# Kernel optimization log

Measured on AMD Instinct MI355X. Metric: run time of the kernel, lower is better.

## Reference

```python
import jax, jax.numpy as jnp
import numpy as np

PAD = 0  # module-level global in the original repo (MT convention)


def setup_inputs() -> dict:
    key = jax.random.key(0)
    k1, k2, k3 = jax.random.split(key, 3)
    N, V, D = 2048, 32000, 512
    # realistic log-probabilities over the vocab
    pred_ll = jax.nn.log_softmax(jax.random.normal(k1, (N, V), jnp.float32), axis=-1)
    target = jax.random.randint(k2, (N,), 0, V)
    # frozen pretrained word-vector table (nn.Embedding.from_pretrained)
    emb = jax.random.normal(k3, (V, D), jnp.float32)
    return {"pred_ll": pred_ll, "target": target, "emb": emb}


def reference(pred_ll, target, emb):
    # pred_ll: [N, V] log-probs; target: [N] int ids; emb: [V, D] frozen table
    mask = (target != PAD).astype(pred_ll.dtype)  # [N] non-pad mask

    # nll_loss = -pred_ll.gather(-1, target) summed over non-pad tokens
    nll = -jnp.take_along_axis(pred_ll, target[:, None], axis=-1)[:, 0]  # [N]
    nll_loss = jnp.sum(nll * mask)

    # pairwise L2 distance gold-embedding vs full table, via the GEMM identity
    # ||g - e||^2 = ||g||^2 + ||e||^2 - 2 g.e  (avoids the [N, V, D] tensor)
    g = emb[target]                                    # [N, D]
    g2 = jnp.sum(g * g, axis=-1, keepdims=True)        # [N, 1]
    e2 = jnp.sum(emb * emb, axis=-1)[None, :]          # [1, V]
    d2 = jnp.maximum(g2 + e2 - 2.0 * (g @ emb.T), 0.0)  # [N, V]
    dist = jnp.sqrt(jnp.maximum(d2, 1e-12))             # [N, V], L2 distances

    dist_max = jnp.max(dist, axis=1, keepdims=True)    # [N, 1]
    w = jax.nn.softmax(dist_max - jnp.abs(dist), axis=1)  # [N, V]

    # loss = sum_v softmax_weight * (-log p), summed over non-pad tokens
    loss = jnp.sum(w * (-pred_ll), axis=1)             # [N]
    return (jnp.sum(loss * mask), nll_loss)
```

## Files before the change

kernel.cpp:

```cpp
#include <hip/hip_runtime.h>
#include <float.h>

#define NTOK   2048
#define VOCAB  32000
#define DIM    512
#define NCHUNK 50
#define NT16   2000
#define TPC    (NT16 / NCHUNK)
#define VCHUNK (VOCAB / NCHUNK)
#define ROWSB  64
#define NRB    (NTOK / ROWSB)
#define TILE_BYTES 8192

typedef __attribute__((ext_vector_type(4))) float f32x4;
typedef unsigned int u32;
typedef long long i64;

__device__ __forceinline__ i64 pack_fp8x8(f32x4 x0, f32x4 x1) {
    int lo = __builtin_amdgcn_cvt_pk_fp8_f32(x0.x, x0.y, 0, false);
    lo = __builtin_amdgcn_cvt_pk_fp8_f32(x0.z, x0.w, lo, true);
    int hi = __builtin_amdgcn_cvt_pk_fp8_f32(x1.x, x1.y, 0, false);
    hi = __builtin_amdgcn_cvt_pk_fp8_f32(x1.z, x1.w, hi, true);
    return (i64)(((unsigned long long)(u32)hi << 32) | (u32)lo);
}

__device__ __forceinline__ void async_copy16(void* lds, const void* g) {
    __builtin_amdgcn_global_load_lds(
        (const __attribute__((address_space(1))) u32*)(const u32*)g,
        (__attribute__((address_space(3))) u32*)(u32*)lds, 16, 0, 0);
}

__global__ void init_out(float* out) {
    if (threadIdx.x < 2) out[threadIdx.x] = 0.f;
}

__global__ __launch_bounds__(256) void precast_kernel(
    const float* __restrict__ emb, char* __restrict__ Bbf, float* __restrict__ e2) {
    const int tile = blockIdx.x;
    const int t = threadIdx.x, w = t >> 6, l = t & 63;
    const int v0 = tile * 16;
    char* tbase = Bbf + (size_t)tile * TILE_BYTES;
    #pragma unroll
    for (int it = 0; it < 4; ++it) {
        const int v = it * 4 + w;
        const float* src = emb + (size_t)(v0 + v) * DIM + l * 8;
        f32x4 x0 = *(const f32x4*)src;
        f32x4 x1 = *(const f32x4*)(src + 4);
        float sq = x0.x*x0.x + x0.y*x0.y + x0.z*x0.z + x0.w*x0.w
                 + x1.x*x1.x + x1.y*x1.y + x1.z*x1.z + x1.w*x1.w;
        #pragma unroll
        for (int m = 1; m < 64; m <<= 1) sq += __shfl_xor(sq, m);
        if (l == 0) e2[v0 + v] = sq;
        *(i64*)(tbase + (l >> 2) * 512 + ((l & 3) * 16 + v) * 8) = pack_fp8x8(x0, x1);
    }
}

__global__ __launch_bounds__(256) void e2_kernel(const float* __restrict__ emb,
                                                 float* __restrict__ e2) {
    int gid = blockIdx.x * 256 + threadIdx.x;
    int wid = gid >> 6, l = gid & 63;
    if (wid >= VOCAB) return;
    const float* row = emb + (size_t)wid * DIM + l * 8;
    f32x4 a = *(const f32x4*)row;
    f32x4 b = *(const f32x4*)(row + 4);
    float s = a.x*a.x + a.y*a.y + a.z*a.z + a.w*a.w
            + b.x*b.x + b.y*b.y + b.z*b.z + b.w*b.w;
    #pragma unroll
    for (int m = 1; m < 64; m <<= 1) s += __shfl_xor(s, m);
    if (l == 0) e2[wid] = s;
}

template<bool PRECAST>
__global__ __launch_bounds__(256, 4) void fused_kernel(
    const float* __restrict__ pred_ll, const int* __restrict__ target,
    const float* __restrict__ emb, const char* __restrict__ Bbf,
    const float* __restrict__ e2g,
    float* __restrict__ partials ) {

    const int rb = blockIdx.x;
    const int ch = blockIdx.y;
    const int t  = threadIdx.x;
    const int w  = t >> 6;
    const int l  = t & 63;
    const int l15 = l & 15;
    const int lg  = l >> 4;

    __shared__ __align__(16) char  ldsB[3][TILE_BYTES];
    __shared__ __align__(16) char  ldsQ[3][4096];
    __shared__ __align__(16) float e2l[VCHUNK];

    const int t0 = ch * TPC, tend = t0 + TPC;
    const int v0base = ch * VCHUNK;
    const int rowblk = rb * ROWSB;
    const int rowbase = rowblk + w * 16;

    i64 afrag[16];
    {
        const int grow = target[rowbase + l15];
        if constexpr (PRECAST) {
            const char* ab = Bbf + (size_t)(grow >> 4) * TILE_BYTES
                           + ((l & 48) + (grow & 15)) * 8;
            #pragma unroll
            for (int ks = 0; ks < 16; ++ks)
                afrag[ks] = *(const i64*)(ab + ks * 512);
        } else {
            const float* gsrc = emb + (size_t)grow * DIM;
            #pragma unroll
            for (int ks = 0; ks < 16; ++ks) {
                const int k0 = ks * 32 + ((l >> 4) << 3);
                afrag[ks] = pack_fp8x8(*(const f32x4*)(gsrc + k0),
                                       *(const f32x4*)(gsrc + k0 + 4));
            }
        }
    }
    float g2[4];
    #pragma unroll
    for (int r = 0; r < 4; ++r) g2[r] = e2g[target[rowbase + lg * 4 + r]];

    float s_[4] = {0.f, 0.f, 0.f, 0.f};
    float ac_[4] = {0.f, 0.f, 0.f, 0.f};

    auto stageF = [&](int buf, int tg) {
        if constexpr (PRECAST) {
            const char* srcB = Bbf + (size_t)tg * TILE_BYTES;
            async_copy16(ldsB[buf] + t * 16, srcB + t * 16);
            async_copy16(ldsB[buf] + 4096 + t * 16, srcB + 4096 + t * 16);
        } else {
            #pragma unroll
            for (int it = 0; it < 4; ++it) {
                const int slot = it * 256 + t;
                const int ks = slot >> 6, il = slot & 63;
                const int v = il & 15, k0 = ks * 32 + ((il >> 4) << 3);
                const float* src = emb + (size_t)(tg * 16 + v) * DIM + k0;
                *(i64*)(ldsB[buf] + ks * 512 + il * 8) =
                    pack_fp8x8(*(const f32x4*)src, *(const f32x4*)(src + 4));
            }
        }
        const float* srcQ = pred_ll + (size_t)(rowblk + (t >> 2)) * VOCAB
                          + tg * 16 + (t & 3) * 4;
        async_copy16(ldsQ[buf] + t * 16, srcQ);
    };

    if (t < VCHUNK / 4) async_copy16(e2l + t * 4, e2g + v0base + t * 4);
    stageF(0, t0);
    stageF(1, t0 + 1);

    int ibr = 0;
    #pragma unroll 1
    for (int tg = t0; tg < tend; ++tg) {
        if (tg == tend - 1) {
            asm volatile("s_waitcnt vmcnt(0)" ::: "memory");
        } else {
            if constexpr (PRECAST)
                asm volatile("s_waitcnt vmcnt(3)" ::: "memory");
            else
                asm volatile("s_waitcnt vmcnt(1) lgkmcnt(0)" ::: "memory");
        }
        __builtin_amdgcn_s_barrier();
        __builtin_amdgcn_sched_barrier(0);

        const int ibw = (ibr >= 1) ? ibr - 1 : ibr + 2;
        if (tg + 2 < tend) stageF(ibw, tg + 2);

        f32x4 acc = {0.f, 0.f, 0.f, 0.f};
        const char* lb = ldsB[ibr];
        #pragma unroll
        for (int ks = 0; ks < 16; ++ks) {
            const i64 b = *(const i64*)(lb + ks * 512 + l * 8);
            acc = __builtin_amdgcn_mfma_f32_16x16x32_fp8_fp8(afrag[ks], b, acc, 0, 0, 0);
        }

        const float e2v = e2l[(tg - t0) * 16 + l15];
        const char* lq = ldsQ[ibr];
        #pragma unroll
        for (int r = 0; r < 4; ++r) {
            const float q = *(const float*)(lq + ((w * 16 + lg * 4 + r) * 64 + l15 * 4));
            float d2 = fmaxf(fmaf(-2.f, acc[r], g2[r] + e2v), 1e-12f);
            const float e = __expf(-sqrtf(d2));
            s_[r] += e;
            ac_[r] = fmaf(e, -q, ac_[r]);
        }

        ibr = (ibr >= 2) ? 0 : ibr + 1;
    }

    #pragma unroll
    for (int r = 0; r < 4; ++r) {
        float sv = s_[r], av = ac_[r];
        #pragma unroll
        for (int m = 1; m < 16; m <<= 1) {
            sv += __shfl_xor(sv, m);
            av += __shfl_xor(av, m);
        }
        if (l15 == 0) {
            const int rg = rowbase + lg * 4 + r;
            float* pp = partials + ((size_t)rg * NCHUNK + ch) * 2;
            pp[0] = sv; pp[1] = av;
        }
    }
}

__global__ __launch_bounds__(256) void reduce_kernel(
    const float* __restrict__ pred_ll, const int* __restrict__ target,
    const float* __restrict__ partials, float* __restrict__ out) {
    const int row = blockIdx.x * 256 + threadIdx.x;
    float loss = 0.f, nll = 0.f;
    if (row < NTOK) {
        const int tg = target[row];
        const float mask = (tg != 0) ? 1.f : 0.f;
        const float* pp = partials + (size_t)row * NCHUNK * 2;
        float S = 0.f, A = 0.f;
        #pragma unroll 5
        for (int c = 0; c < NCHUNK; ++c) { S += pp[c * 2]; A += pp[c * 2 + 1]; }
        loss = mask * (A / S);
        nll  = mask * (-pred_ll[(size_t)row * VOCAB + tg]);
    }
    #pragma unroll
    for (int o = 32; o > 0; o >>= 1) {
        loss += __shfl_xor(loss, o);
        nll  += __shfl_xor(nll, o);
    }
    if ((threadIdx.x & 63) == 0) {
        atomicAdd(&out[0], loss);
        atomicAdd(&out[1], nll);
    }
}

extern "C" void kernel_launch(void* const* d_in, const int* in_sizes, int n_in,
                              void* d_out, int out_size, void* d_ws, size_t ws_size,
                              hipStream_t stream) {
    const float* pred_ll = (const float*)d_in[0];
    const int*   target  = (const int*)d_in[1];
    const float* emb     = (const float*)d_in[2];
    float* out = (float*)d_out;

    float* e2       = (float*)d_ws;
    float* partials = e2 + VOCAB;
    const size_t base = (size_t)VOCAB * 4 + (size_t)NTOK * NCHUNK * 2 * 4;
    char* Bbf       = (char*)d_ws + base;
    const size_t need = base + (size_t)NT16 * TILE_BYTES;
    const bool precast = (ws_size >= need);

    hipLaunchKernelGGL(init_out, dim3(1), dim3(64), 0, stream, out);
    if (precast) {
        hipLaunchKernelGGL(precast_kernel, dim3(NT16), dim3(256), 0, stream, emb, Bbf, e2);
        hipLaunchKernelGGL((fused_kernel<true>), dim3(NRB, NCHUNK), dim3(256), 0, stream,
                           pred_ll, target, emb, Bbf, e2, partials);
    } else {
        hipLaunchKernelGGL(e2_kernel, dim3(VOCAB * 64 / 256), dim3(256), 0, stream, emb, e2);
        hipLaunchKernelGGL((fused_kernel<false>), dim3(NRB, NCHUNK), dim3(256), 0, stream,
                           pred_ll, target, emb, Bbf, e2, partials);
    }
    hipLaunchKernelGGL(reduce_kernel, dim3(NTOK / 256), dim3(256), 0, stream,
                       pred_ll, target, partials, out);
}
```

Before: 173.5 us.

## Restructure fused kernel pipeline with 5-deep B buffers and register-staged Q superblocks

```diff
diff --git a/kernel.cpp b/kernel.cpp
--- a/kernel.cpp
+++ b/kernel.cpp
@@ -6,8 +6,8 @@
 #define DIM    512
 #define NCHUNK 50
 #define NT16   2000
-#define TPC    (NT16 / NCHUNK)
-#define VCHUNK (VOCAB / NCHUNK)
+#define TPC    40
+#define NSUP   5
 #define ROWSB  64
 #define NRB    (NTOK / ROWSB)
 #define TILE_BYTES 8192
@@ -15,6 +15,8 @@
 typedef __attribute__((ext_vector_type(4))) float f32x4;
 typedef unsigned int u32;
 typedef long long i64;
+
+template<int N> struct IC { static constexpr int v = N; };
 
 __device__ __forceinline__ i64 pack_fp8x8(f32x4 x0, f32x4 x1) {
     int lo = __builtin_amdgcn_cvt_pk_fp8_f32(x0.x, x0.y, 0, false);
@@ -71,7 +73,7 @@
 }
 
 template<bool PRECAST>
-__global__ __launch_bounds__(256, 4) void fused_kernel(
+__global__ __launch_bounds__(256, 2) void fused_kernel(
     const float* __restrict__ pred_ll, const int* __restrict__ target,
     const float* __restrict__ emb, const char* __restrict__ Bbf,
     const float* __restrict__ e2g,
@@ -85,12 +87,11 @@
     const int l15 = l & 15;
     const int lg  = l >> 4;
 
-    __shared__ __align__(16) char  ldsB[3][TILE_BYTES];
-    __shared__ __align__(16) char  ldsQ[3][4096];
-    __shared__ __align__(16) float e2l[VCHUNK];
-
-    const int t0 = ch * TPC, tend = t0 + TPC;
-    const int v0base = ch * VCHUNK;
+    __shared__ __align__(16) char  ldsB[5][TILE_BYTES];
+    __shared__ __align__(16) float ldsQ[64 * 128];
+    __shared__ __align__(16) float e2l[1024];
+
+    const int t0 = ch * TPC;
     const int rowblk = rb * ROWSB;
     const int rowbase = rowblk + w * 16;
 
@@ -120,68 +121,127 @@
     float s_[4] = {0.f, 0.f, 0.f, 0.f};
     float ac_[4] = {0.f, 0.f, 0.f, 0.f};
 
-    auto stageF = [&](int buf, int tg) {
-        if constexpr (PRECAST) {
-            const char* srcB = Bbf + (size_t)tg * TILE_BYTES;
-            async_copy16(ldsB[buf] + t * 16, srcB + t * 16);
-            async_copy16(ldsB[buf] + 4096 + t * 16, srcB + 4096 + t * 16);
-        } else {
+    if constexpr (!PRECAST) {
+        for (int g = t0; g < t0 + TPC; ++g) {
+            __syncthreads();
             #pragma unroll
             for (int it = 0; it < 4; ++it) {
-                const int slot = it * 256 + t;
-                const int ks = slot >> 6, il = slot & 63;
+                const int slot = it * 256 + t, ks = slot >> 6, il = slot & 63;
                 const int v = il & 15, k0 = ks * 32 + ((il >> 4) << 3);
-                const float* src = emb + (size_t)(tg * 16 + v) * DIM + k0;
-                *(i64*)(ldsB[buf] + ks * 512 + il * 8) =
+                const float* src = emb + (size_t)(g * 16 + v) * DIM + k0;
+                *(i64*)(ldsB[0] + ks * 512 + il * 8) =
                     pack_fp8x8(*(const f32x4*)src, *(const f32x4*)(src + 4));
             }
-        }
-        const float* srcQ = pred_ll + (size_t)(rowblk + (t >> 2)) * VOCAB
-                          + tg * 16 + (t & 3) * 4;
-        async_copy16(ldsQ[buf] + t * 16, srcQ);
-    };
-
-    if (t < VCHUNK / 4) async_copy16(e2l + t * 4, e2g + v0base + t * 4);
-    stageF(0, t0);
-    stageF(1, t0 + 1);
-
-    int ibr = 0;
-    #pragma unroll 1
-    for (int tg = t0; tg < tend; ++tg) {
-        if (tg == tend - 1) {
-            asm volatile("s_waitcnt vmcnt(0)" ::: "memory");
-        } else {
-            if constexpr (PRECAST)
-                asm volatile("s_waitcnt vmcnt(3)" ::: "memory");
-            else
-                asm volatile("s_waitcnt vmcnt(1) lgkmcnt(0)" ::: "memory");
-        }
-        __builtin_amdgcn_s_barrier();
-        __builtin_amdgcn_sched_barrier(0);
-
-        const int ibw = (ibr >= 1) ? ibr - 1 : ibr + 2;
-        if (tg + 2 < tend) stageF(ibw, tg + 2);
-
-        f32x4 acc = {0.f, 0.f, 0.f, 0.f};
-        const char* lb = ldsB[ibr];
-        #pragma unroll
-        for (int ks = 0; ks < 16; ++ks) {
-            const i64 b = *(const i64*)(lb + ks * 512 + l * 8);
-            acc = __builtin_amdgcn_mfma_f32_16x16x32_fp8_fp8(afrag[ks], b, acc, 0, 0, 0);
-        }
-
-        const float e2v = e2l[(tg - t0) * 16 + l15];
-        const char* lq = ldsQ[ibr];
-        #pragma unroll
-        for (int r = 0; r < 4; ++r) {
-            const float q = *(const float*)(lq + ((w * 16 + lg * 4 + r) * 64 + l15 * 4));
-            float d2 = fmaxf(fmaf(-2.f, acc[r], g2[r] + e2v), 1e-12f);
-            const float e = __expf(-sqrtf(d2));
-            s_[r] += e;
-            ac_[r] = fmaf(e, -q, ac_[r]);
-        }
-
-        ibr = (ibr >= 2) ? 0 : ibr + 1;
+            __syncthreads();
+            f32x4 acc = {0.f, 0.f, 0.f, 0.f};
+            #pragma unroll
+            for (int ks = 0; ks < 16; ++ks) {
+                const i64 bb = *(const i64*)(ldsB[0] + ks * 512 + l * 8);
+                acc = __builtin_amdgcn_mfma_f32_16x16x32_fp8_fp8(afrag[ks], bb, acc, 0, 0, 0);
+            }
+            const float e2v = e2g[g * 16 + l15];
+            #pragma unroll
+            for (int r = 0; r < 4; ++r) {
+                const float q = pred_ll[(size_t)(rowbase + lg * 4 + r) * VOCAB + g * 16 + l15];
+                float d2 = fmaxf(fmaf(-2.f, acc[r], g2[r] + e2v), 1e-12f);
+                const float e = __expf(-sqrtf(d2));
+                s_[r] += e;
+                ac_[r] = fmaf(e, -q, ac_[r]);
+            }
+        }
+    } else {
+        float qreg[4][8];
+
+        auto stageQ = [&](int k) {
+            const int colf = (t0 + k * 8) * 16;
+            #pragma unroll
+            for (int j = 0; j < 8; ++j) {
+                const int f = j * 256 + t;
+                async_copy16((char*)ldsQ + (size_t)(j * 4096 + t * 16),
+                             pred_ll + (size_t)(rowblk + (f >> 5)) * VOCAB
+                                     + colf + (f & 31) * 4);
+            }
+        };
+        auto stageB = [&](int g) {
+            char* dst = ldsB[(g - t0) % 5];
+            const char* src = Bbf + (size_t)g * TILE_BYTES;
+            async_copy16(dst + t * 16, src + t * 16);
+            async_copy16(dst + 4096 + t * 16, src + 4096 + t * 16);
+        };
+
+        asm volatile("s_waitcnt vmcnt(0)" ::: "memory");
+
+        {
+            int src = ch * (TPC * 16) + t * 4;
+            if (src > VOCAB - 4) src = VOCAB - 4;
+            async_copy16(e2l + t * 4, e2g + src);
+        }
+        stageQ(0);
+        stageB(t0); stageB(t0 + 1); stageB(t0 + 2); stageB(t0 + 3);
+
+        auto step = [&](int b, auto Iw, auto Xw, auto Dw) {
+            constexpr int i = decltype(Iw)::v;
+            constexpr int X = decltype(Xw)::v;
+            constexpr bool D = decltype(Dw)::v != 0;
+            const int g = b + i;
+            asm volatile("s_waitcnt vmcnt(%0)" :: "i"(X) : "memory");
+            __builtin_amdgcn_s_barrier();
+            __builtin_amdgcn_sched_barrier(0);
+            if constexpr (D) stageB(g + 4);
+            const char* lb = ldsB[(g - t0) % 5];
+            f32x4 acc = {0.f, 0.f, 0.f, 0.f};
+            #pragma unroll
+            for (int ks = 0; ks < 16; ++ks) {
+                const i64 bb = *(const i64*)(lb + ks * 512 + l * 8);
+                acc = __builtin_amdgcn_mfma_f32_16x16x32_fp8_fp8(afrag[ks], bb, acc, 0, 0, 0);
+            }
+            const float e2v = e2l[(g - t0) * 16 + l15];
+            #pragma unroll
+            for (int r = 0; r < 4; ++r) {
+                float d2 = fmaxf(fmaf(-2.f, acc[r], g2[r] + e2v), 1e-12f);
+                const float e = __expf(-sqrtf(d2));
+                s_[r] += e;
+                ac_[r] = fmaf(e, -qreg[r][i], ac_[r]);
+            }
+        };
+
+        auto boundary = [&](int k) {
+            asm volatile("s_waitcnt vmcnt(8)" ::: "memory");
+            #pragma unroll
+            for (int r = 0; r < 4; ++r)
+                #pragma unroll
+                for (int i = 0; i < 8; ++i)
+                    qreg[r][i] = ldsQ[(w * 16 + lg * 4 + r) * 128 + i * 16 + l15];
+            asm volatile("s_waitcnt lgkmcnt(0)" ::: "memory");
+            __builtin_amdgcn_s_barrier();
+            if (k + 1 < NSUP) stageQ(k + 1);
+        };
+
+        #pragma unroll 1
+        for (int k = 0; k < NSUP - 1; ++k) {
+            const int b = t0 + k * 8;
+            boundary(k);
+            step(b, IC<0>{}, IC<14>{}, IC<1>{});
+            step(b, IC<1>{}, IC<14>{}, IC<1>{});
+            step(b, IC<2>{}, IC<14>{}, IC<1>{});
+            step(b, IC<3>{}, IC<14>{}, IC<1>{});
+            step(b, IC<4>{}, IC<6>{},  IC<1>{});
+            step(b, IC<5>{}, IC<6>{},  IC<1>{});
+            step(b, IC<6>{}, IC<6>{},  IC<1>{});
+            step(b, IC<7>{}, IC<6>{},  IC<1>{});
+        }
+        {
+            const int b = t0 + (NSUP - 1) * 8;
+            boundary(NSUP - 1);
+            step(b, IC<0>{}, IC<6>{}, IC<1>{});
+            step(b, IC<1>{}, IC<6>{}, IC<1>{});
+            step(b, IC<2>{}, IC<6>{}, IC<1>{});
+            step(b, IC<3>{}, IC<6>{}, IC<1>{});
+            step(b, IC<4>{}, IC<6>{}, IC<0>{});
+            step(b, IC<5>{}, IC<4>{}, IC<0>{});
+            step(b, IC<6>{}, IC<2>{}, IC<0>{});
+            step(b, IC<7>{}, IC<0>{}, IC<0>{});
+        }
     }
 
     #pragma unroll
```

Measured after the change: 218.3 us. +25.8%, slower.
